# Performance work log

Hardware: AMD Instinct MI355X
Metric: run time of the kernel (lower is better)

## Reference

```python
import jax, jax.numpy as jnp
import numpy as np
from jax import tree_util as jtu

B, N, DIM = 2, 2048, 512
HEADS, DH = 4, 128
CHUNK = 64
NC = N // CHUNK
DHID = 4 * DH  # expansion_factor 4
MAX_LR = 1.0   # default_step_transform_max_lr


def rms_norm(x, g, eps=1e-6):
    var = jnp.mean(jnp.square(x), axis=-1, keepdims=True)
    return x * jax.lax.rsqrt(var + eps) * g


def mem_model(params, x):
    # ResidualNorm(MemoryMLP depth=2): out = mlp(rmsnorm(x)) + x
    g, w1, w2 = params
    h = rms_norm(x, g)
    h = jax.nn.gelu(jnp.dot(h, w1), approximate=False)
    h = jnp.dot(h, w2)
    return h + x


def _expand(a, leaf):
    # broadcast a per-(b*h) scalar gate over a weight leaf
    return a.reshape(a.shape + (1,) * (leaf.ndim - 1))


def neural_memory(seq, g_store, g_retrieve, Wq, Wk, Wv, Wa, ba, Wm, Wd, bd, Wg, Wc, mem_g, w1, w2):
    xs = rms_norm(seq, g_store)      # store_norm
    xr = rms_norm(seq, g_retrieve)   # retrieve_norm

    def split_heads(t):
        return t.reshape(B, N, HEADS, DH).transpose(0, 2, 1, 3)  # b h n d

    k = split_heads(xs @ Wk)
    v = split_heads(xs @ Wv)
    q = split_heads(xr @ Wq)

    # adaptive per-token lr (sigmoid * max_lr)
    lr = (jax.nn.sigmoid(xs @ Wa + ba) * MAX_LR).transpose(0, 2, 1)  # [B,H,N]
    # per-chunk pooled stats drive momentum + decay gates (AveragePool)
    pooled = xs.reshape(B, NC, CHUNK, DIM).mean(axis=2)              # [B,NC,DIM]
    beta = jax.nn.sigmoid(pooled @ Wm)                               # momentum factor [B,NC,H]
    alpha = 1.0 - jax.nn.sigmoid(pooled @ Wd + bd)                   # weight-retain (1-decay)

    BH = B * HEADS
    k_c = k.reshape(BH, NC, CHUNK, DH)
    v_c = v.reshape(BH, NC, CHUNK, DH)
    q_c = q.reshape(BH, NC, CHUNK, DH)
    lr_c = lr.reshape(BH, NC, CHUNK)
    beta_t = beta.transpose(0, 2, 1).reshape(BH, NC).T   # [NC,BH]
    alpha_t = alpha.transpose(0, 2, 1).reshape(BH, NC).T

    # per-head memory params repeated over batch*heads (per_head_learned_parameters)
    init_params = (
        jnp.broadcast_to(mem_g, (B, HEADS, DH)).reshape(BH, DH),
        jnp.broadcast_to(w1, (B, HEADS, DH, DHID)).reshape(BH, DH, DHID),
        jnp.broadcast_to(w2, (B, HEADS, DHID, DH)).reshape(BH, DHID, DH),
    )

    def chunk_loss(params, kc, vc, lrc):
        pred = mem_model(params, kc)                              # [CHUNK,DH]
        return jnp.sum(jnp.mean(jnp.square(pred - vc), axis=-1) * lrc)

    # per-chunk 'surprise' gradients: vmap over (b*h) and chunks, grads wrt init weights
    grad_fn = jax.grad(chunk_loss)
    grads = jax.vmap(jax.vmap(grad_fn, in_axes=(None, 0, 0, 0)), in_axes=(0, 0, 0, 0))(
        init_params, k_c, v_c, lr_c)
    sur_t = jtu.tree_map(lambda g: jnp.moveaxis(-g, 1, 0), grads)  # [NC,BH,...]

    # momentum recurrence: m_t = beta_t * m_{t-1} + surprise_t
    def mom_step(m, inp):
        b, s = inp
        m = jtu.tree_map(lambda mm, ss: _expand(b, mm) * mm + ss, m, s)
        return m, m
    m0 = jtu.tree_map(lambda t: jnp.zeros_like(t[0]), sur_t)
    _, upd_t = jax.lax.scan(mom_step, m0, (beta_t, sur_t))

    # weight recurrence with decay: w_t = (1-decay_t) * w_{t-1} + m_t
    def w_step(w, inp):
        a, u = inp
        w = jtu.tree_map(lambda ww, uu: _expand(a, ww) * ww + uu, w, u)
        return w, w
    _, w_t = jax.lax.scan(w_step, init_params, (alpha_t, upd_t))

    # causal retrieval: chunk i reads weights updated through chunk i-1
    w_prev = jtu.tree_map(
        lambda wt, w0: jnp.moveaxis(jnp.concatenate([w0[None], wt[:-1]], axis=0), 0, 1),
        w_t, init_params)                                          # [BH,NC,...]

    retrieved = jax.vmap(jax.vmap(mem_model))(w_prev, q_c)         # [BH,NC,CHUNK,DH]
    retrieved = retrieved.reshape(B, HEADS, N, DH)
    gate = jax.nn.sigmoid(xr @ Wg).transpose(0, 2, 1)[..., None]   # retrieve_gate [B,H,N,1]
    retrieved = retrieved * gate
    out = retrieved.transpose(0, 2, 1, 3).reshape(B, N, HEADS * DH) @ Wc  # combine_heads
    return out


def setup_inputs():
    key = jax.random.key(0)
    ks = jax.random.split(key, 12)
    s = 0.02
    f = jnp.float32
    return {
        "seq": jax.random.normal(ks[0], (B, N, DIM), f),
        "g_store": jnp.ones((DIM,), f),
        "g_retrieve": jnp.ones((DIM,), f),
        "Wq": jax.random.normal(ks[1], (DIM, HEADS * DH), f) * s,
        "Wk": jax.random.normal(ks[2], (DIM, HEADS * DH), f) * s,
        "Wv": jax.random.normal(ks[3], (DIM, HEADS * DH), f) * s,
        "Wa": jax.random.normal(ks[4], (DIM, HEADS), f) * s,
        "ba": jnp.zeros((HEADS,), f),
        "Wm": jax.random.normal(ks[5], (DIM, HEADS), f) * s,
        "Wd": jax.random.normal(ks[6], (DIM, HEADS), f) * s,
        "bd": jnp.zeros((HEADS,), f),
        "Wg": jax.random.normal(ks[7], (DIM, HEADS), f) * s,
        "Wc": jax.random.normal(ks[8], (HEADS * DH, DIM), f) * s,
        "mem_g": jnp.ones((DH,), f),
        "w1": jax.random.normal(ks[9], (DH, DHID), f) * (1.0 / np.sqrt(DH)),
        "w2": jax.random.normal(ks[10], (DHID, DH), f) * (1.0 / np.sqrt(DHID)),
    }


def reference(seq, g_store, g_retrieve, Wq, Wk, Wv, Wa, ba, Wm, Wd, bd, Wg, Wc, mem_g, w1, w2):
    return neural_memory(seq, g_store, g_retrieve, Wq, Wk, Wv, Wa, ba, Wm, Wd, bd, Wg, Wc, mem_g, w1, w2)
```

## Files before the change

### kernel.cpp

```cpp
#include <hip/hip_runtime.h>
#include <hip/hip_bf16.h>

#define B_ 2
#define N_ 2048
#define DIM_ 512
#define H_ 4
#define DH_ 128
#define DHID_ 512
#define CH_ 64
#define NC_ 32
#define BH_ 8

typedef __bf16 bf16x8 __attribute__((ext_vector_type(8)));
typedef float f32x4 __attribute__((ext_vector_type(4)));

__device__ __forceinline__ f32x4 MFMA(bf16x8 a, bf16x8 b, f32x4 c) {
    return __builtin_amdgcn_mfma_f32_16x16x32_bf16(a, b, c, 0, 0, 0);
}
__device__ __forceinline__ bf16x8 ld8(const __bf16* p) { return *(const bf16x8*)p; }

__device__ __forceinline__ float sigmoidf_(float x) { return 1.0f / (1.0f + expf(-x)); }
__device__ __forceinline__ float gelu_f(float x) {
    return x * 0.5f * (1.0f + erff(x * 0.7071067811865476f));
}
__device__ __forceinline__ float gelu_g(float x) {
    float cdf = 0.5f * (1.0f + erff(x * 0.7071067811865476f));
    float pdf = 0.3989422804014327f * expf(-0.5f * x * x);
    return cdf + x * pdf;
}

__global__ __launch_bounds__(256) void rms_kernel(
    const float* __restrict__ seq, const float* __restrict__ gs,
    const float* __restrict__ gr, float* __restrict__ xs, float* __restrict__ xr,
    __bf16* __restrict__ xsb, __bf16* __restrict__ xrb)
{
    const int row = blockIdx.x;
    const int t = threadIdx.x;
    const float* x = seq + (size_t)row * DIM_;
    float v0 = x[t], v1 = x[t + 256];
    float ss = v0 * v0 + v1 * v1;
#pragma unroll
    for (int off = 32; off; off >>= 1) ss += __shfl_xor(ss, off);
    __shared__ float red[4];
    if ((t & 63) == 0) red[t >> 6] = ss;
    __syncthreads();
    float tot = red[0] + red[1] + red[2] + red[3];
    float r = rsqrtf(tot * (1.0f / DIM_) + 1e-6f);
    size_t o = (size_t)row * DIM_;
    float a0 = v0 * r * gs[t], a1 = v1 * r * gs[t + 256];
    float b0 = v0 * r * gr[t], b1 = v1 * r * gr[t + 256];
    xs[o + t] = a0; xs[o + t + 256] = a1;
    xr[o + t] = b0; xr[o + t + 256] = b1;
    xsb[o + t] = (__bf16)a0; xsb[o + t + 256] = (__bf16)a1;
    xrb[o + t] = (__bf16)b0; xrb[o + t + 256] = (__bf16)b1;
}

__global__ __launch_bounds__(256) void pooled_kernel(
    const float* __restrict__ xs, float* __restrict__ pooled)
{
    int idx = blockIdx.x * 256 + threadIdx.x;
    int d = idx & 511;
    int ci = (idx >> 9) & 31;
    int b = idx >> 14;
    const float* base = xs + ((size_t)b * N_ + ci * CH_) * DIM_ + d;
    float s = 0.f;
#pragma unroll 8
    for (int c = 0; c < CH_; ++c) s += base[(size_t)c * DIM_];
    pooled[idx] = s * (1.0f / CH_);
}

__global__ __launch_bounds__(256) void gates_kernel(
    const float* __restrict__ xs, const float* __restrict__ xr,
    const float* __restrict__ Wa, const float* __restrict__ ba,
    const float* __restrict__ Wg, float* __restrict__ lrb, float* __restrict__ gateb)
{
    const int t = threadIdx.x;
    const int wave = t >> 6, lane = t & 63;
    const int row = blockIdx.x * 4 + wave;
    const int b = row >> 11, n = row & 2047;
    const float* xsr = xs + (size_t)row * DIM_;
    const float* xrr = xr + (size_t)row * DIM_;
#pragma unroll
    for (int h = 0; h < H_; ++h) {
        float aA = 0.f, aG = 0.f;
        for (int d = lane; d < DIM_; d += 64) {
            aA += xsr[d] * Wa[d * H_ + h];
            aG += xrr[d] * Wg[d * H_ + h];
        }
#pragma unroll
        for (int off = 32; off; off >>= 1) {
            aA += __shfl_xor(aA, off);
            aG += __shfl_xor(aG, off);
        }
        if (lane == 0) {
            int bh = b * H_ + h;
            lrb[(size_t)bh * N_ + n] = sigmoidf_(aA + ba[h]);
            gateb[(size_t)bh * N_ + n] = sigmoidf_(aG);
        }
    }
}

__global__ __launch_bounds__(256) void ba_kernel(
    const float* __restrict__ pooled, const float* __restrict__ Wm,
    const float* __restrict__ Wd, const float* __restrict__ bd,
    float* __restrict__ beta, float* __restrict__ alpha)
{
    const int t = threadIdx.x;
    const int b = t >> 7, rem = t & 127, ci = rem >> 2, h = rem & 3;
    const float* p = pooled + ((size_t)b * NC_ + ci) * DIM_;
    float am = 0.f, ad = 0.f;
    for (int d = 0; d < DIM_; ++d) {
        float pv = p[d];
        am += pv * Wm[d * H_ + h];
        ad += pv * Wd[d * H_ + h];
    }
    int bh = b * H_ + h;
    beta[bh * NC_ + ci] = sigmoidf_(am);
    alpha[bh * NC_ + ci] = 1.0f - sigmoidf_(ad + bd[h]);
}

__global__ __launch_bounds__(256) void prep_kernel(
    const float* __restrict__ w1, const float* __restrict__ w2,
    const float* __restrict__ Wq, const float* __restrict__ Wk,
    const float* __restrict__ Wv, const float* __restrict__ Wc,
    __bf16* __restrict__ w1b, __bf16* __restrict__ w1Tb,
    __bf16* __restrict__ w2b, __bf16* __restrict__ w2Tb,
    __bf16* __restrict__ WqT, __bf16* __restrict__ WkT,
    __bf16* __restrict__ WvT, __bf16* __restrict__ WcT)
{
    int idx = blockIdx.x * 256 + threadIdx.x;
    if (idx < 65536) {
        w1b[idx] = (__bf16)w1[idx];
        int j = idx >> 7, d = idx & 127;
        w1Tb[idx] = (__bf16)w1[(size_t)d * DHID_ + j];
        w2b[idx] = (__bf16)w2[idx];
        int d2 = idx >> 9, j2 = idx & 511;
        w2Tb[idx] = (__bf16)w2[(size_t)j2 * DH_ + d2];
    }
    int n = idx >> 9, k = idx & 511;
    WqT[idx] = (__bf16)Wq[(size_t)k * 512 + n];
    WkT[idx] = (__bf16)Wk[(size_t)k * 512 + n];
    WvT[idx] = (__bf16)Wv[(size_t)k * 512 + n];
    WcT[idx] = (__bf16)Wc[(size_t)k * 512 + n];
}

template <int SPLIT>
__global__ __launch_bounds__(256, 4) void gemm_bf(
    const __bf16* __restrict__ A, const __bf16* __restrict__ WT, float* __restrict__ out)
{
    const int t = threadIdx.x;
    const int wave = t >> 6, lane = t & 63;
    const int lrow = lane & 15, lgrp = lane >> 4;
    const int c0 = blockIdx.x * 64 + wave * 16;
    const int col0 = blockIdx.y * 64;
    f32x4 acc[4];
#pragma unroll
    for (int i = 0; i < 4; ++i) acc[i] = (f32x4)0.f;
    const __bf16* ar = A + (size_t)(c0 + lrow) * 512;
#pragma unroll 4
    for (int k0 = 0; k0 < 512; k0 += 32) {
        bf16x8 av = ld8(ar + k0 + lgrp * 8);
#pragma unroll
        for (int ct = 0; ct < 4; ++ct) {
            bf16x8 bv = ld8(WT + (size_t)(col0 + ct * 16 + lrow) * 512 + k0 + lgrp * 8);
            acc[ct] = MFMA(av, bv, acc[ct]);
        }
    }
#pragma unroll
    for (int ct = 0; ct < 4; ++ct)
#pragma unroll
        for (int r = 0; r < 4; ++r) {
            int row = c0 + lgrp * 4 + r, col = col0 + ct * 16 + lrow;
            if (SPLIT) {
                int b = row >> 11, n = row & 2047, h = col >> 7, d = col & 127;
                out[((((size_t)(b * H_ + h) * NC_ + (n >> 6)) * CH_) + (n & 63)) * DH_ + d] = acc[ct][r];
            } else {
                out[(size_t)row * 512 + col] = acc[ct][r];
            }
        }
}

__global__ __launch_bounds__(512, 2) void grad_kernel(
    const float* __restrict__ kbuf, const float* __restrict__ vbuf,
    const float* __restrict__ lrbuf, const float* __restrict__ memg,
    const __bf16* __restrict__ w1b, const __bf16* __restrict__ w1Tb,
    const __bf16* __restrict__ w2b, const __bf16* __restrict__ w2Tb,
    float* __restrict__ sg, __bf16* __restrict__ sw1, __bf16* __restrict__ sw2)
{
    const int blk = blockIdx.x;
    const int t = threadIdx.x;
    const int w = t >> 6, lane = t & 63;
    const int lrow = lane & 15, lgrp = lane >> 4;
    const int bh = blk >> 5, nc = blk & 31;
    const float* kc = kbuf + (size_t)blk * (CH_ * DH_);
    const float* vc = vbuf + (size_t)blk * (CH_ * DH_);
    const float* lrp = lrbuf + (size_t)bh * N_ + nc * CH_;
    __bf16* sw1_blk = sw1 + (size_t)blk * (DHID_ * DH_);
    __bf16* sw2_blk = sw2 + (size_t)blk * (DHID_ * DH_);

    __shared__ __bf16 h_s[64][136];
    __shared__ __bf16 e_s[64][136];
    __shared__ __bf16 a_s[64][136];
    __shared__ __bf16 dz_s[64][136];
    __shared__ __bf16 hT_s[128][72];
    __shared__ __bf16 eT_s[128][72];
    __shared__ __bf16 aT_s[128][72];
    __shared__ __bf16 dzT_s[128][72];
    __shared__ float r_s[64];
    __shared__ float lr_s[64];
    __shared__ float g_s[128];

    if (t < 128) g_s[t] = memg[t];
    if (t < 64) lr_s[t] = lrp[t];
    {
        const int c = t >> 3, dblk = t & 7, d0 = dblk * 16;
        float xv[16];
        float ss = 0.f;
#pragma unroll
        for (int i = 0; i < 4; ++i) {
            float4 f = *(const float4*)(kc + (size_t)c * DH_ + d0 + i * 4);
            xv[i * 4 + 0] = f.x; xv[i * 4 + 1] = f.y; xv[i * 4 + 2] = f.z; xv[i * 4 + 3] = f.w;
            ss += f.x * f.x + f.y * f.y + f.z * f.z + f.w * f.w;
        }
        ss += __shfl_xor(ss, 1); ss += __shfl_xor(ss, 2); ss += __shfl_xor(ss, 4);
        float r = rsqrtf(ss * (1.0f / DH_) + 1e-6f);
        if (dblk == 0) r_s[c] = r;
        __syncthreads();
#pragma unroll
        for (int i = 0; i < 16; ++i)
            h_s[c][d0 + i] = (__bf16)(xv[i] * r * g_s[d0 + i]);
    }
    __syncthreads();
    {
        const int d = t >> 2, c0 = (t & 3) * 16;
#pragma unroll
        for (int i = 0; i < 16; ++i) hT_s[d][c0 + i] = h_s[c0 + i][d];
    }
    __syncthreads();

    const int cs = w & 3, half = w >> 2;
    const int c0w = cs * 16, off64 = half * 64;
    f32x4 yacc[4];
#pragma unroll
    for (int i = 0; i < 4; ++i) yacc[i] = (f32x4)0.f;

    for (int jt = 0; jt < 4; ++jt) {
        f32x4 zacc[4];
#pragma unroll
        for (int i = 0; i < 4; ++i) zacc[i] = (f32x4)0.f;
#pragma unroll
        for (int kt = 0; kt < 4; ++kt) {
            bf16x8 av = ld8(&h_s[c0w + lrow][kt * 32 + lgrp * 8]);
#pragma unroll
            for (int ct = 0; ct < 4; ++ct) {
                int j = jt * 128 + off64 + ct * 16 + lrow;
                bf16x8 bv = ld8(w1Tb + (size_t)j * 128 + kt * 32 + lgrp * 8);
                zacc[ct] = MFMA(av, bv, zacc[ct]);
            }
        }
#pragma unroll
        for (int ct = 0; ct < 4; ++ct)
#pragma unroll
            for (int r = 0; r < 4; ++r)
                a_s[c0w + lgrp * 4 + r][off64 + ct * 16 + lrow] = (__bf16)gelu_f(zacc[ct][r]);
        __syncthreads();
#pragma unroll
        for (int kt = 0; kt < 4; ++kt) {
            bf16x8 av = ld8(&a_s[c0w + lrow][kt * 32 + lgrp * 8]);
#pragma unroll
            for (int ct = 0; ct < 4; ++ct) {
                int d = off64 + ct * 16 + lrow;
                bf16x8 bv = ld8(w2Tb + (size_t)d * 512 + jt * 128 + kt * 32 + lgrp * 8);
                yacc[ct] = MFMA(av, bv, yacc[ct]);
            }
        }
        __syncthreads();
    }
#pragma unroll
    for (int ct = 0; ct < 4; ++ct)
#pragma unroll
        for (int r = 0; r < 4; ++r) {
            int c = c0w + lgrp * 4 + r, d = off64 + ct * 16 + lrow;
            float xvv = kc[(size_t)c * DH_ + d];
            float vvv = vc[(size_t)c * DH_ + d];
            float e = lr_s[c] * (2.0f / DH_) * (yacc[ct][r] + xvv - vvv);
            e_s[c][d] = (__bf16)e;
            eT_s[d][c] = (__bf16)e;
        }
    __syncthreads();

    const int jl0 = w * 16;
    f32x4 dhacc[4];
#pragma unroll
    for (int i = 0; i < 4; ++i) dhacc[i] = (f32x4)0.f;

    for (int jt = 0; jt < 4; ++jt) {
        f32x4 ztacc[4], dtacc[4];
#pragma unroll
        for (int i = 0; i < 4; ++i) { ztacc[i] = (f32x4)0.f; dtacc[i] = (f32x4)0.f; }
#pragma unroll
        for (int kt = 0; kt < 4; ++kt) {
            bf16x8 avz = ld8(w1Tb + (size_t)(jt * 128 + jl0 + lrow) * 128 + kt * 32 + lgrp * 8);
            bf16x8 avd = ld8(w2b  + (size_t)(jt * 128 + jl0 + lrow) * 128 + kt * 32 + lgrp * 8);
#pragma unroll
            for (int ct = 0; ct < 4; ++ct) {
                bf16x8 bvh = ld8(&h_s[ct * 16 + lrow][kt * 32 + lgrp * 8]);
                bf16x8 bve = ld8(&e_s[ct * 16 + lrow][kt * 32 + lgrp * 8]);
                ztacc[ct] = MFMA(avz, bvh, ztacc[ct]);
                dtacc[ct] = MFMA(avd, bve, dtacc[ct]);
            }
        }
#pragma unroll
        for (int ct = 0; ct < 4; ++ct)
#pragma unroll
            for (int r = 0; r < 4; ++r) {
                int j = jl0 + lgrp * 4 + r, c = ct * 16 + lrow;
                float zt = ztacc[ct][r];
                aT_s[j][c] = (__bf16)gelu_f(zt);
                float dzt = dtacc[ct][r] * gelu_g(zt);
                dzT_s[j][c] = (__bf16)dzt;
                dz_s[c][j] = (__bf16)dzt;
            }
        __syncthreads();
        {
            f32x4 wacc[8];
#pragma unroll
            for (int i = 0; i < 8; ++i) wacc[i] = (f32x4)0.f;
#pragma unroll
            for (int kt = 0; kt < 2; ++kt) {
                bf16x8 av = ld8(&dzT_s[jl0 + lrow][kt * 32 + lgrp * 8]);
#pragma unroll
                for (int ct = 0; ct < 8; ++ct) {
                    bf16x8 bv = ld8(&hT_s[ct * 16 + lrow][kt * 32 + lgrp * 8]);
                    wacc[ct] = MFMA(av, bv, wacc[ct]);
                }
            }
#pragma unroll
            for (int ct = 0; ct < 8; ++ct)
#pragma unroll
                for (int r = 0; r < 4; ++r) {
                    int jg = jt * 128 + jl0 + lgrp * 4 + r, d = ct * 16 + lrow;
                    sw1_blk[(size_t)jg * 128 + d] = (__bf16)(-wacc[ct][r]);
                }
        }
        {
            f32x4 wacc[8];
#pragma unroll
            for (int i = 0; i < 8; ++i) wacc[i] = (f32x4)0.f;
#pragma unroll
            for (int kt = 0; kt < 2; ++kt) {
                bf16x8 av = ld8(&eT_s[jl0 + lrow][kt * 32 + lgrp * 8]);
#pragma unroll
                for (int ct = 0; ct < 8; ++ct) {
                    bf16x8 bv = ld8(&aT_s[ct * 16 + lrow][kt * 32 + lgrp * 8]);
                    wacc[ct] = MFMA(av, bv, wacc[ct]);
                }
            }
#pragma unroll
            for (int ct = 0; ct < 8; ++ct)
#pragma unroll
                for (int r = 0; r < 4; ++r) {
                    int d = jl0 + lgrp * 4 + r, jg = jt * 128 + ct * 16 + lrow;
                    sw2_blk[(size_t)d * 512 + jg] = (__bf16)(-wacc[ct][r]);
                }
        }
#pragma unroll
        for (int kt = 0; kt < 4; ++kt) {
            bf16x8 av = ld8(w1b + (size_t)(jl0 + lrow) * 512 + jt * 128 + kt * 32 + lgrp * 8);
#pragma unroll
            for (int ct = 0; ct < 4; ++ct) {
                bf16x8 bv = ld8(&dz_s[ct * 16 + lrow][kt * 32 + lgrp * 8]);
                dhacc[ct] = MFMA(av, bv, dhacc[ct]);
            }
        }
        __syncthreads();
    }
    {
        float s[4] = {0.f, 0.f, 0.f, 0.f};
#pragma unroll
        for (int ct = 0; ct < 4; ++ct)
#pragma unroll
            for (int r = 0; r < 4; ++r) {
                int d = jl0 + lgrp * 4 + r, c = ct * 16 + lrow;
                s[r] += dhacc[ct][r] * (float)hT_s[d][c];
            }
#pragma unroll
        for (int r = 0; r < 4; ++r) {
            s[r] += __shfl_xor(s[r], 1); s[r] += __shfl_xor(s[r], 2);
            s[r] += __shfl_xor(s[r], 4); s[r] += __shfl_xor(s[r], 8);
        }
        if (lrow == 0) {
#pragma unroll
            for (int r = 0; r < 4; ++r) {
                int d = jl0 + lgrp * 4 + r;
                sg[(size_t)blk * DH_ + d] = -s[r] / g_s[d];
            }
        }
    }
}

__global__ __launch_bounds__(256) void scan_bf(
    __bf16* __restrict__ buf, const __bf16* __restrict__ init,
    const float* __restrict__ beta, const float* __restrict__ alpha)
{
    int idx = blockIdx.x * 256 + threadIdx.x;
    int bh = idx >> 16, el = idx & 65535;
    float wv = (float)init[el], m = 0.f;
    const float* bp = beta + bh * NC_;
    const float* ap = alpha + bh * NC_;
    __bf16* base = buf + ((size_t)bh * NC_) * 65536 + el;
    for (int ci = 0; ci < NC_; ++ci) {
        float s = (float)base[(size_t)ci * 65536];
        base[(size_t)ci * 65536] = (__bf16)wv;
        m = fmaf(bp[ci], m, s);
        wv = fmaf(ap[ci], wv, m);
    }
}

__global__ __launch_bounds__(256) void scan_g(
    float* __restrict__ buf, const float* __restrict__ init,
    const float* __restrict__ beta, const float* __restrict__ alpha)
{
    int idx = blockIdx.x * 256 + threadIdx.x;
    int bh = idx >> 7, el = idx & 127;
    float wv = init[el], m = 0.f;
    const float* bp = beta + bh * NC_;
    const float* ap = alpha + bh * NC_;
    float* base = buf + ((size_t)bh * NC_) * 128 + el;
    for (int ci = 0; ci < NC_; ++ci) {
        float s = base[(size_t)ci * 128];
        base[(size_t)ci * 128] = wv;
        m = fmaf(bp[ci], m, s);
        wv = fmaf(ap[ci], wv, m);
    }
}

__global__ __launch_bounds__(256, 2) void retrieve_kernel(
    const float* __restrict__ qbuf, const float* __restrict__ gatebuf,
    const float* __restrict__ sg, const __bf16* __restrict__ sw1,
    const __bf16* __restrict__ sw2, __bf16* __restrict__ retgb)
{
    const int blk = blockIdx.x;
    const int t = threadIdx.x;
    const int w = t >> 6, lane = t & 63;
    const int lrow = lane & 15, lgrp = lane >> 4;
    const int bh = blk >> 5, nc = blk & 31;
    const float* qc = qbuf + (size_t)blk * (CH_ * DH_);
    const __bf16* w1p = sw1 + (size_t)blk * (DHID_ * DH_);
    const __bf16* w2p = sw2 + (size_t)blk * (DHID_ * DH_);
    const float* gp = sg + (size_t)blk * DH_;

    __shared__ __bf16 h_s[64][136];
    __shared__ __bf16 a_s[64][136];
    __shared__ float g_s[128];

    if (t < 128) g_s[t] = gp[t];
    {
        const int c = t >> 2, dblk = t & 3, d0 = dblk * 32;
        float xv[32];
        float ss = 0.f;
#pragma unroll
        for (int i = 0; i < 8; ++i) {
            float4 f = *(const float4*)(qc + (size_t)c * DH_ + d0 + i * 4);
            xv[i * 4 + 0] = f.x; xv[i * 4 + 1] = f.y; xv[i * 4 + 2] = f.z; xv[i * 4 + 3] = f.w;
            ss += f.x * f.x + f.y * f.y + f.z * f.z + f.w * f.w;
        }
        ss += __shfl_xor(ss, 1); ss += __shfl_xor(ss, 2);
        float r = rsqrtf(ss * (1.0f / DH_) + 1e-6f);
        __syncthreads();
#pragma unroll
        for (int i = 0; i < 32; ++i)
            h_s[c][d0 + i] = (__bf16)(xv[i] * r * g_s[d0 + i]);
    }
    __syncthreads();

    const int c0w = w * 16;
    f32x4 yacc[8];
#pragma unroll
    for (int i = 0; i < 8; ++i) yacc[i] = (f32x4)0.f;

    for (int jt = 0; jt < 4; ++jt) {
        f32x4 zacc[8];
#pragma unroll
        for (int i = 0; i < 8; ++i) zacc[i] = (f32x4)0.f;
#pragma unroll
        for (int kt = 0; kt < 4; ++kt) {
            bf16x8 av = ld8(&h_s[c0w + lrow][kt * 32 + lgrp * 8]);
#pragma unroll
            for (int ct = 0; ct < 8; ++ct) {
                int j = jt * 128 + ct * 16 + lrow;
                bf16x8 bv = ld8(w1p + (size_t)j * 128 + kt * 32 + lgrp * 8);
                zacc[ct] = MFMA(av, bv, zacc[ct]);
            }
        }
#pragma unroll
        for (int ct = 0; ct < 8; ++ct)
#pragma unroll
            for (int r = 0; r < 4; ++r)
                a_s[c0w + lgrp * 4 + r][ct * 16 + lrow] = (__bf16)gelu_f(zacc[ct][r]);
        __syncthreads();
#pragma unroll
        for (int kt = 0; kt < 4; ++kt) {
            bf16x8 av = ld8(&a_s[c0w + lrow][kt * 32 + lgrp * 8]);
#pragma unroll
            for (int ct = 0; ct < 8; ++ct) {
                int d = ct * 16 + lrow;
                bf16x8 bv = ld8(w2p + (size_t)d * 512 + jt * 128 + kt * 32 + lgrp * 8);
                yacc[ct] = MFMA(av, bv, yacc[ct]);
            }
        }
        __syncthreads();
    }
    const int b = bh >> 2, hh = bh & 3;
#pragma unroll
    for (int ct = 0; ct < 8; ++ct)
#pragma unroll
        for (int r = 0; r < 4; ++r) {
            int c = c0w + lgrp * 4 + r, d = ct * 16 + lrow;
            int n = nc * CH_ + c;
            float q = qc[(size_t)c * DH_ + d];
            float gv = gatebuf[(size_t)bh * N_ + n];
            retgb[((size_t)(b * N_ + n)) * 512 + hh * 128 + d] = (__bf16)((yacc[ct][r] + q) * gv);
        }
}

extern "C" void kernel_launch(void* const* d_in, const int* in_sizes, int n_in,
                              void* d_out, int out_size, void* d_ws, size_t ws_size,
                              hipStream_t stream) {
    const float* seq     = (const float*)d_in[0];
    const float* g_store = (const float*)d_in[1];
    const float* g_retr  = (const float*)d_in[2];
    const float* Wq = (const float*)d_in[3];
    const float* Wk = (const float*)d_in[4];
    const float* Wv = (const float*)d_in[5];
    const float* Wa = (const float*)d_in[6];
    const float* ba = (const float*)d_in[7];
    const float* Wm = (const float*)d_in[8];
    const float* Wd = (const float*)d_in[9];
    const float* bd = (const float*)d_in[10];
    const float* Wg = (const float*)d_in[11];
    const float* Wc = (const float*)d_in[12];
    const float* memg = (const float*)d_in[13];
    const float* w1 = (const float*)d_in[14];
    const float* w2 = (const float*)d_in[15];
    float* out = (float*)d_out;

    float* p = (float*)d_ws;
    float* xs = p;     p += (size_t)B_ * N_ * DIM_;
    float* xr = p;     p += (size_t)B_ * N_ * DIM_;
    float* kb = p;     p += (size_t)B_ * N_ * DIM_;
    float* vb = p;     p += (size_t)B_ * N_ * DIM_;
    float* qb = p;     p += (size_t)B_ * N_ * DIM_;
    float* lrb = p;    p += (size_t)BH_ * N_;
    float* gateb = p;  p += (size_t)BH_ * N_;
    float* pooled = p; p += (size_t)B_ * NC_ * DIM_;
    float* beta = p;   p += BH_ * NC_;
    float* alpha = p;  p += BH_ * NC_;
    float* sgb = p;    p += (size_t)BH_ * NC_ * DH_;

    __bf16* bp_ = (__bf16*)p;
    __bf16* xsb = bp_;  bp_ += (size_t)B_ * N_ * DIM_;
    __bf16* xrb = bp_;  bp_ += (size_t)B_ * N_ * DIM_;
    __bf16* retgb = bp_; bp_ += (size_t)B_ * N_ * DIM_;
    __bf16* w1b = bp_;  bp_ += DH_ * DHID_;
    __bf16* w1Tb = bp_; bp_ += DH_ * DHID_;
    __bf16* w2b = bp_;  bp_ += DH_ * DHID_;
    __bf16* w2Tb = bp_; bp_ += DH_ * DHID_;
    __bf16* WqT = bp_;  bp_ += DIM_ * DIM_;
    __bf16* WkT = bp_;  bp_ += DIM_ * DIM_;
    __bf16* WvT = bp_;  bp_ += DIM_ * DIM_;
    __bf16* WcT = bp_;  bp_ += DIM_ * DIM_;
    __bf16* sw1b = bp_; bp_ += (size_t)BH_ * NC_ * DH_ * DHID_;
    __bf16* sw2b = bp_; bp_ += (size_t)BH_ * NC_ * DH_ * DHID_;

    rms_kernel<<<B_ * N_, 256, 0, stream>>>(seq, g_store, g_retr, xs, xr, xsb, xrb);
    pooled_kernel<<<(B_ * NC_ * DIM_) / 256, 256, 0, stream>>>(xs, pooled);
    gates_kernel<<<(B_ * N_) / 4, 256, 0, stream>>>(xs, xr, Wa, ba, Wg, lrb, gateb);
    ba_kernel<<<1, 256, 0, stream>>>(pooled, Wm, Wd, bd, beta, alpha);
    prep_kernel<<<1024, 256, 0, stream>>>(w1, w2, Wq, Wk, Wv, Wc,
                                          w1b, w1Tb, w2b, w2Tb, WqT, WkT, WvT, WcT);
    gemm_bf<1><<<dim3(64, 8), 256, 0, stream>>>(xrb, WqT, qb);
    gemm_bf<1><<<dim3(64, 8), 256, 0, stream>>>(xsb, WkT, kb);
    gemm_bf<1><<<dim3(64, 8), 256, 0, stream>>>(xsb, WvT, vb);
    grad_kernel<<<BH_ * NC_, 512, 0, stream>>>(kb, vb, lrb, memg, w1b, w1Tb, w2b, w2Tb,
                                               sgb, sw1b, sw2b);
    scan_bf<<<(BH_ * 65536) / 256, 256, 0, stream>>>(sw1b, w1Tb, beta, alpha);
    scan_bf<<<(BH_ * 65536) / 256, 256, 0, stream>>>(sw2b, w2Tb, beta, alpha);
    scan_g<<<(BH_ * DH_) / 256, 256, 0, stream>>>(sgb, memg, beta, alpha);
    retrieve_kernel<<<BH_ * NC_, 256, 0, stream>>>(qb, gateb, sgb, sw1b, sw2b, retgb);
    gemm_bf<0><<<dim3(64, 8), 256, 0, stream>>>(retgb, WcT, out);
}
```

Before: 387.2 us.

## Fuse small kernels and double threads per block in grad and retrieve

Folds the lr/gate projections into the RMS-norm kernel, and merges the pooling with the beta/alpha gates into one kernel that runs on 64 blocks instead of one. The three QKV GEMMs become one launch over a z grid dimension, and the three scan launches become one. grad_kernel moves from 512 to 1024 threads and retrieve_kernel from 256 to 512, with each wave taking a smaller tile so only 256 blocks spread more work across waves. This cuts launch count and raises per-block parallelism, at the cost of more per-thread register pressure limits and extra synchronisation.

```diff
diff --git a/kernel.cpp b/kernel.cpp
--- a/kernel.cpp
+++ b/kernel.cpp
@@ -31,18 +31,23 @@
 
 __global__ __launch_bounds__(256) void rms_kernel(
     const float* __restrict__ seq, const float* __restrict__ gs,
-    const float* __restrict__ gr, float* __restrict__ xs, float* __restrict__ xr,
-    __bf16* __restrict__ xsb, __bf16* __restrict__ xrb)
+    const float* __restrict__ gr, const float* __restrict__ Wa,
+    const float* __restrict__ ba, const float* __restrict__ Wg,
+    float* __restrict__ xs, float* __restrict__ xr,
+    __bf16* __restrict__ xsb, __bf16* __restrict__ xrb,
+    float* __restrict__ lrb, float* __restrict__ gateb)
 {
     const int row = blockIdx.x;
     const int t = threadIdx.x;
+    const int wave = t >> 6, lane = t & 63;
     const float* x = seq + (size_t)row * DIM_;
     float v0 = x[t], v1 = x[t + 256];
     float ss = v0 * v0 + v1 * v1;
 #pragma unroll
     for (int off = 32; off; off >>= 1) ss += __shfl_xor(ss, off);
     __shared__ float red[4];
-    if ((t & 63) == 0) red[t >> 6] = ss;
+    __shared__ float red2[4][8];
+    if (lane == 0) red[wave] = ss;
     __syncthreads();
     float tot = red[0] + red[1] + red[2] + red[3];
     float r = rsqrtf(tot * (1.0f / DIM_) + 1e-6f);
@@ -53,70 +58,81 @@
     xr[o + t] = b0; xr[o + t + 256] = b1;
     xsb[o + t] = (__bf16)a0; xsb[o + t + 256] = (__bf16)a1;
     xrb[o + t] = (__bf16)b0; xrb[o + t + 256] = (__bf16)b1;
-}
-
-__global__ __launch_bounds__(256) void pooled_kernel(
-    const float* __restrict__ xs, float* __restrict__ pooled)
-{
-    int idx = blockIdx.x * 256 + threadIdx.x;
-    int d = idx & 511;
-    int ci = (idx >> 9) & 31;
-    int b = idx >> 14;
-    const float* base = xs + ((size_t)b * N_ + ci * CH_) * DIM_ + d;
-    float s = 0.f;
-#pragma unroll 8
-    for (int c = 0; c < CH_; ++c) s += base[(size_t)c * DIM_];
-    pooled[idx] = s * (1.0f / CH_);
-}
-
-__global__ __launch_bounds__(256) void gates_kernel(
-    const float* __restrict__ xs, const float* __restrict__ xr,
-    const float* __restrict__ Wa, const float* __restrict__ ba,
-    const float* __restrict__ Wg, float* __restrict__ lrb, float* __restrict__ gateb)
-{
+    float pa[4], pg[4];
+#pragma unroll
+    for (int h = 0; h < 4; ++h) {
+        pa[h] = a0 * Wa[t * 4 + h] + a1 * Wa[(t + 256) * 4 + h];
+        pg[h] = b0 * Wg[t * 4 + h] + b1 * Wg[(t + 256) * 4 + h];
+    }
+#pragma unroll
+    for (int h = 0; h < 4; ++h)
+#pragma unroll
+        for (int off = 32; off; off >>= 1) {
+            pa[h] += __shfl_xor(pa[h], off);
+            pg[h] += __shfl_xor(pg[h], off);
+        }
+    if (lane == 0) {
+#pragma unroll
+        for (int h = 0; h < 4; ++h) {
+            red2[wave][h] = pa[h];
+            red2[wave][4 + h] = pg[h];
+        }
+    }
+    __syncthreads();
+    if (t < 8) {
+        float s = red2[0][t] + red2[1][t] + red2[2][t] + red2[3][t];
+        int b = row >> 11, n = row & 2047;
+        if (t < 4) lrb[(size_t)(b * 4 + t) * N_ + n] = sigmoidf_(s + ba[t]);
+        else gateb[(size_t)(b * 4 + (t - 4)) * N_ + n] = sigmoidf_(s);
+    }
+}
+
+__global__ __launch_bounds__(256) void ba_kernel(
+    const float* __restrict__ xs, const float* __restrict__ Wm,
+    const float* __restrict__ Wd, const float* __restrict__ bd,
+    float* __restrict__ beta, float* __restrict__ alpha)
+{
+    const int b = blockIdx.x >> 5, ci = blockIdx.x & 31;
     const int t = threadIdx.x;
     const int wave = t >> 6, lane = t & 63;
-    const int row = blockIdx.x * 4 + wave;
-    const int b = row >> 11, n = row & 2047;
-    const float* xsr = xs + (size_t)row * DIM_;
-    const float* xrr = xr + (size_t)row * DIM_;
-#pragma unroll
-    for (int h = 0; h < H_; ++h) {
-        float aA = 0.f, aG = 0.f;
-        for (int d = lane; d < DIM_; d += 64) {
-            aA += xsr[d] * Wa[d * H_ + h];
-            aG += xrr[d] * Wg[d * H_ + h];
-        }
+    const float* base = xs + ((size_t)b * N_ + ci * CH_) * DIM_;
+    const int d0 = t * 2;
+    float s0 = 0.f, s1 = 0.f;
+#pragma unroll 8
+    for (int r = 0; r < CH_; ++r) {
+        s0 += base[(size_t)r * DIM_ + d0];
+        s1 += base[(size_t)r * DIM_ + d0 + 1];
+    }
+    s0 *= (1.0f / CH_); s1 *= (1.0f / CH_);
+    float pm[4], pd[4];
+#pragma unroll
+    for (int h = 0; h < 4; ++h) {
+        pm[h] = s0 * Wm[d0 * 4 + h] + s1 * Wm[(d0 + 1) * 4 + h];
+        pd[h] = s0 * Wd[d0 * 4 + h] + s1 * Wd[(d0 + 1) * 4 + h];
+    }
+#pragma unroll
+    for (int h = 0; h < 4; ++h)
 #pragma unroll
         for (int off = 32; off; off >>= 1) {
-            aA += __shfl_xor(aA, off);
-            aG += __shfl_xor(aG, off);
-        }
-        if (lane == 0) {
-            int bh = b * H_ + h;
-            lrb[(size_t)bh * N_ + n] = sigmoidf_(aA + ba[h]);
-            gateb[(size_t)bh * N_ + n] = sigmoidf_(aG);
-        }
-    }
-}
-
-__global__ __launch_bounds__(256) void ba_kernel(
-    const float* __restrict__ pooled, const float* __restrict__ Wm,
-    const float* __restrict__ Wd, const float* __restrict__ bd,
-    float* __restrict__ beta, float* __restrict__ alpha)
-{
-    const int t = threadIdx.x;
-    const int b = t >> 7, rem = t & 127, ci = rem >> 2, h = rem & 3;
-    const float* p = pooled + ((size_t)b * NC_ + ci) * DIM_;
-    float am = 0.f, ad = 0.f;
-    for (int d = 0; d < DIM_; ++d) {
-        float pv = p[d];
-        am += pv * Wm[d * H_ + h];
-        ad += pv * Wd[d * H_ + h];
-    }
-    int bh = b * H_ + h;
-    beta[bh * NC_ + ci] = sigmoidf_(am);
-    alpha[bh * NC_ + ci] = 1.0f - sigmoidf_(ad + bd[h]);
+            pm[h] += __shfl_xor(pm[h], off);
+            pd[h] += __shfl_xor(pd[h], off);
+        }
+    __shared__ float red2[4][8];
+    if (lane == 0) {
+#pragma unroll
+        for (int h = 0; h < 4; ++h) {
+            red2[wave][h] = pm[h];
+            red2[wave][4 + h] = pd[h];
+        }
+    }
+    __syncthreads();
+    if (t < 4) {
+        float sm = red2[0][t] + red2[1][t] + red2[2][t] + red2[3][t];
+        float sd = red2[0][4 + t] + red2[1][4 + t] + red2[2][4 + t] + red2[3][4 + t];
+        int bh = b * 4 + t;
+        beta[bh * NC_ + ci] = sigmoidf_(sm);
+        alpha[bh * NC_ + ci] = 1.0f - sigmoidf_(sd + bd[t]);
+    }
 }
 
 __global__ __launch_bounds__(256) void prep_kernel(
@@ -144,10 +160,16 @@
     WcT[idx] = (__bf16)Wc[(size_t)k * 512 + n];
 }
 
-template <int SPLIT>
-__global__ __launch_bounds__(256, 4) void gemm_bf(
-    const __bf16* __restrict__ A, const __bf16* __restrict__ WT, float* __restrict__ out)
-{
+__global__ __launch_bounds__(256, 4) void proj_kernel(
+    const __bf16* __restrict__ xsb, const __bf16* __restrict__ xrb,
+    const __bf16* __restrict__ WqT, const __bf16* __restrict__ WkT,
+    const __bf16* __restrict__ WvT,
+    float* __restrict__ qb, float* __restrict__ kb, float* __restrict__ vb)
+{
+    const int z = blockIdx.z;
+    const __bf16* A = (z == 0) ? xrb : xsb;
+    const __bf16* WT = (z == 0) ? WqT : (z == 1 ? WkT : WvT);
+    float* out = (z == 0) ? qb : (z == 1 ? kb : vb);
     const int t = threadIdx.x;
     const int wave = t >> 6, lane = t & 63;
     const int lrow = lane & 15, lgrp = lane >> 4;
@@ -171,16 +193,42 @@
 #pragma unroll
         for (int r = 0; r < 4; ++r) {
             int row = c0 + lgrp * 4 + r, col = col0 + ct * 16 + lrow;
-            if (SPLIT) {
-                int b = row >> 11, n = row & 2047, h = col >> 7, d = col & 127;
-                out[((((size_t)(b * H_ + h) * NC_ + (n >> 6)) * CH_) + (n & 63)) * DH_ + d] = acc[ct][r];
-            } else {
-                out[(size_t)row * 512 + col] = acc[ct][r];
-            }
-        }
-}
-
-__global__ __launch_bounds__(512, 2) void grad_kernel(
+            int b = row >> 11, n = row & 2047, h = col >> 7, d = col & 127;
+            out[((((size_t)(b * H_ + h) * NC_ + (n >> 6)) * CH_) + (n & 63)) * DH_ + d] = acc[ct][r];
+        }
+}
+
+__global__ __launch_bounds__(256, 4) void gemm_out(
+    const __bf16* __restrict__ A, const __bf16* __restrict__ WT, float* __restrict__ out)
+{
+    const int t = threadIdx.x;
+    const int wave = t >> 6, lane = t & 63;
+    const int lrow = lane & 15, lgrp = lane >> 4;
+    const int c0 = blockIdx.x * 64 + wave * 16;
+    const int col0 = blockIdx.y * 64;
+    f32x4 acc[4];
+#pragma unroll
+    for (int i = 0; i < 4; ++i) acc[i] = (f32x4)0.f;
+    const __bf16* ar = A + (size_t)(c0 + lrow) * 512;
+#pragma unroll 4
+    for (int k0 = 0; k0 < 512; k0 += 32) {
+        bf16x8 av = ld8(ar + k0 + lgrp * 8);
+#pragma unroll
+        for (int ct = 0; ct < 4; ++ct) {
+            bf16x8 bv = ld8(WT + (size_t)(col0 + ct * 16 + lrow) * 512 + k0 + lgrp * 8);
+            acc[ct] = MFMA(av, bv, acc[ct]);
+        }
+    }
+#pragma unroll
+    for (int ct = 0; ct < 4; ++ct)
+#pragma unroll
+        for (int r = 0; r < 4; ++r) {
+            int row = c0 + lgrp * 4 + r, col = col0 + ct * 16 + lrow;
+            out[(size_t)row * 512 + col] = acc[ct][r];
+        }
+}
+
+__global__ __launch_bounds__(1024) void grad_kernel(
     const float* __restrict__ kbuf, const float* __restrict__ vbuf,
     const float* __restrict__ lrbuf, const float* __restrict__ memg,
     const __bf16* __restrict__ w1b, const __bf16* __restrict__ w1Tb,
@@ -209,67 +257,67 @@
     __shared__ float r_s[64];
     __shared__ float lr_s[64];
     __shared__ float g_s[128];
+    __shared__ float part_s[2][128];
 
     if (t < 128) g_s[t] = memg[t];
     if (t < 64) lr_s[t] = lrp[t];
     {
-        const int c = t >> 3, dblk = t & 7, d0 = dblk * 16;
-        float xv[16];
+        const int c = t >> 4, i8 = t & 15, d0 = i8 * 8;
+        float xv[8];
         float ss = 0.f;
 #pragma unroll
-        for (int i = 0; i < 4; ++i) {
+        for (int i = 0; i < 2; ++i) {
             float4 f = *(const float4*)(kc + (size_t)c * DH_ + d0 + i * 4);
             xv[i * 4 + 0] = f.x; xv[i * 4 + 1] = f.y; xv[i * 4 + 2] = f.z; xv[i * 4 + 3] = f.w;
             ss += f.x * f.x + f.y * f.y + f.z * f.z + f.w * f.w;
         }
-        ss += __shfl_xor(ss, 1); ss += __shfl_xor(ss, 2); ss += __shfl_xor(ss, 4);
+        ss += __shfl_xor(ss, 1); ss += __shfl_xor(ss, 2);
+        ss += __shfl_xor(ss, 4); ss += __shfl_xor(ss, 8);
         float r = rsqrtf(ss * (1.0f / DH_) + 1e-6f);
-        if (dblk == 0) r_s[c] = r;
-        __syncthreads();
-#pragma unroll
-        for (int i = 0; i < 16; ++i)
+        if (i8 == 0) r_s[c] = r;
+        __syncthreads();
+#pragma unroll
+        for (int i = 0; i < 8; ++i)
             h_s[c][d0 + i] = (__bf16)(xv[i] * r * g_s[d0 + i]);
     }
     __syncthreads();
     {
-        const int d = t >> 2, c0 = (t & 3) * 16;
-#pragma unroll
-        for (int i = 0; i < 16; ++i) hT_s[d][c0 + i] = h_s[c0 + i][d];
+        const int d = t >> 3, c0 = (t & 7) * 8;
+#pragma unroll
+        for (int i = 0; i < 8; ++i) hT_s[d][c0 + i] = h_s[c0 + i][d];
     }
     __syncthreads();
 
-    const int cs = w & 3, half = w >> 2;
-    const int c0w = cs * 16, off64 = half * 64;
-    f32x4 yacc[4];
-#pragma unroll
-    for (int i = 0; i < 4; ++i) yacc[i] = (f32x4)0.f;
+    const int cs = w & 3, dq = w >> 2;
+    const int c0w = cs * 16, q0 = dq * 32;
+    f32x4 yacc[2];
+    yacc[0] = (f32x4)0.f; yacc[1] = (f32x4)0.f;
 
     for (int jt = 0; jt < 4; ++jt) {
-        f32x4 zacc[4];
-#pragma unroll
-        for (int i = 0; i < 4; ++i) zacc[i] = (f32x4)0.f;
+        f32x4 zacc[2];
+        zacc[0] = (f32x4)0.f; zacc[1] = (f32x4)0.f;
 #pragma unroll
         for (int kt = 0; kt < 4; ++kt) {
             bf16x8 av = ld8(&h_s[c0w + lrow][kt * 32 + lgrp * 8]);
 #pragma unroll
-            for (int ct = 0; ct < 4; ++ct) {
-                int j = jt * 128 + off64 + ct * 16 + lrow;
+            for (int ct = 0; ct < 2; ++ct) {
+                int j = jt * 128 + q0 + ct * 16 + lrow;
                 bf16x8 bv = ld8(w1Tb + (size_t)j * 128 + kt * 32 + lgrp * 8);
                 zacc[ct] = MFMA(av, bv, zacc[ct]);
             }
         }
 #pragma unroll
-        for (int ct = 0; ct < 4; ++ct)
+        for (int ct = 0; ct < 2; ++ct)
 #pragma unroll
             for (int r = 0; r < 4; ++r)
-                a_s[c0w + lgrp * 4 + r][off64 + ct * 16 + lrow] = (__bf16)gelu_f(zacc[ct][r]);
+                a_s[c0w + lgrp * 4 + r][q0 + ct * 16 + lrow] = (__bf16)gelu_f(zacc[ct][r]);
         __syncthreads();
 #pragma unroll
         for (int kt = 0; kt < 4; ++kt) {
             bf16x8 av = ld8(&a_s[c0w + lrow][kt * 32 + lgrp * 8]);
 #pragma unroll
-            for (int ct = 0; ct < 4; ++ct) {
-                int d = off64 + ct * 16 + lrow;
+            for (int ct = 0; ct < 2; ++ct) {
+                int d = q0 + ct * 16 + lrow;
                 bf16x8 bv = ld8(w2Tb + (size_t)d * 512 + jt * 128 + kt * 32 + lgrp * 8);
                 yacc[ct] = MFMA(av, bv, yacc[ct]);
             }
@@ -277,10 +325,10 @@
         __syncthreads();
     }
 #pragma unroll
-    for (int ct = 0; ct < 4; ++ct)
+    for (int ct = 0; ct < 2; ++ct)
 #pragma unroll
         for (int r = 0; r < 4; ++r) {
-            int c = c0w + lgrp * 4 + r, d = off64 + ct * 16 + lrow;
+            int c = c0w + lgrp * 4 + r, d = q0 + ct * 16 + lrow;
             float xvv = kc[(size_t)c * DH_ + d];
             float vvv = vc[(size_t)c * DH_ + d];
             float e = lr_s[c] * (2.0f / DH_) * (yacc[ct][r] + xvv - vvv);
@@ -289,32 +337,31 @@
         }
     __syncthreads();
 
-    const int jl0 = w * 16;
-    f32x4 dhacc[4];
-#pragma unroll
-    for (int i = 0; i < 4; ++i) dhacc[i] = (f32x4)0.f;
+    const int js = w & 7, chh = w >> 3;
+    f32x4 dhacc[2];
+    dhacc[0] = (f32x4)0.f; dhacc[1] = (f32x4)0.f;
 
     for (int jt = 0; jt < 4; ++jt) {
-        f32x4 ztacc[4], dtacc[4];
-#pragma unroll
-        for (int i = 0; i < 4; ++i) { ztacc[i] = (f32x4)0.f; dtacc[i] = (f32x4)0.f; }
+        f32x4 ztacc[2], dtacc[2];
+        ztacc[0] = (f32x4)0.f; ztacc[1] = (f32x4)0.f;
+        dtacc[0] = (f32x4)0.f; dtacc[1] = (f32x4)0.f;
 #pragma unroll
         for (int kt = 0; kt < 4; ++kt) {
-            bf16x8 avz = ld8(w1Tb + (size_t)(jt * 128 + jl0 + lrow) * 128 + kt * 32 + lgrp * 8);
-            bf16x8 avd = ld8(w2b  + (size_t)(jt * 128 + jl0 + lrow) * 128 + kt * 32 + lgrp * 8);
-#pragma unroll
-            for (int ct = 0; ct < 4; ++ct) {
-                bf16x8 bvh = ld8(&h_s[ct * 16 + lrow][kt * 32 + lgrp * 8]);
-                bf16x8 bve = ld8(&e_s[ct * 16 + lrow][kt * 32 + lgrp * 8]);
+            bf16x8 avz = ld8(w1Tb + (size_t)(jt * 128 + js * 16 + lrow) * 128 + kt * 32 + lgrp * 8);
+            bf16x8 avd = ld8(w2b  + (size_t)(jt * 128 + js * 16 + lrow) * 128 + kt * 32 + lgrp * 8);
+#pragma unroll
+            for (int ct = 0; ct < 2; ++ct) {
+                bf16x8 bvh = ld8(&h_s[chh * 32 + ct * 16 + lrow][kt * 32 + lgrp * 8]);
+                bf16x8 bve = ld8(&e_s[chh * 32 + ct * 16 + lrow][kt * 32 + lgrp * 8]);
                 ztacc[ct] = MFMA(avz, bvh, ztacc[ct]);
                 dtacc[ct] = MFMA(avd, bve, dtacc[ct]);
             }
         }
 #pragma unroll
-        for (int ct = 0; ct < 4; ++ct)
+        for (int ct = 0; ct < 2; ++ct)
 #pragma unroll
             for (int r = 0; r < 4; ++r) {
-                int j = jl0 + lgrp * 4 + r, c = ct * 16 + lrow;
+                int j = js * 16 + lgrp * 4 + r, c = chh * 32 + ct * 16 + lrow;
                 float zt = ztacc[ct][r];
                 aT_s[j][c] = (__bf16)gelu_f(zt);
                 float dzt = dtacc[ct][r] * gelu_g(zt);
@@ -323,53 +370,53 @@
             }
         __syncthreads();
         {
-            f32x4 wacc[8];
-#pragma unroll
-            for (int i = 0; i < 8; ++i) wacc[i] = (f32x4)0.f;
+            f32x4 wacc[4];
+#pragma unroll
+            for (int i = 0; i < 4; ++i) wacc[i] = (f32x4)0.f;
 #pragma unroll
             for (int kt = 0; kt < 2; ++kt) {
-                bf16x8 av = ld8(&dzT_s[jl0 + lrow][kt * 32 + lgrp * 8]);
-#pragma unroll
-                for (int ct = 0; ct < 8; ++ct) {
-                    bf16x8 bv = ld8(&hT_s[ct * 16 + lrow][kt * 32 + lgrp * 8]);
+                bf16x8 av = ld8(&dzT_s[js * 16 + lrow][kt * 32 + lgrp * 8]);
+#pragma unroll
+                for (int ct = 0; ct < 4; ++ct) {
+                    bf16x8 bv = ld8(&hT_s[chh * 64 + ct * 16 + lrow][kt * 32 + lgrp * 8]);
                     wacc[ct] = MFMA(av, bv, wacc[ct]);
                 }
             }
 #pragma unroll
-            for (int ct = 0; ct < 8; ++ct)
+            for (int ct = 0; ct < 4; ++ct)
 #pragma unroll
                 for (int r = 0; r < 4; ++r) {
-                    int jg = jt * 128 + jl0 + lgrp * 4 + r, d = ct * 16 + lrow;
+                    int jg = jt * 128 + js * 16 + lgrp * 4 + r, d = chh * 64 + ct * 16 + lrow;
                     sw1_blk[(size_t)jg * 128 + d] = (__bf16)(-wacc[ct][r]);
                 }
         }
         {
-            f32x4 wacc[8];
-#pragma unroll
-            for (int i = 0; i < 8; ++i) wacc[i] = (f32x4)0.f;
+            f32x4 wacc[4];
+#pragma unroll
+            for (int i = 0; i < 4; ++i) wacc[i] = (f32x4)0.f;
 #pragma unroll
             for (int kt = 0; kt < 2; ++kt) {
-                bf16x8 av = ld8(&eT_s[jl0 + lrow][kt * 32 + lgrp * 8]);
-#pragma unroll
-                for (int ct = 0; ct < 8; ++ct) {
-                    bf16x8 bv = ld8(&aT_s[ct * 16 + lrow][kt * 32 + lgrp * 8]);
+                bf16x8 av = ld8(&eT_s[js * 16 + lrow][kt * 32 + lgrp * 8]);
+#pragma unroll
+                for (int ct = 0; ct < 4; ++ct) {
+                    bf16x8 bv = ld8(&aT_s[chh * 64 + ct * 16 + lrow][kt * 32 + lgrp * 8]);
                     wacc[ct] = MFMA(av, bv, wacc[ct]);
                 }
             }
 #pragma unroll
-            for (int ct = 0; ct < 8; ++ct)
+            for (int ct = 0; ct < 4; ++ct)
 #pragma unroll
                 for (int r = 0; r < 4; ++r) {
-                    int d = jl0 + lgrp * 4 + r, jg = jt * 128 + ct * 16 + lrow;
+                    int d = js * 16 + lgrp * 4 + r, jg = jt * 128 + chh * 64 + ct * 16 + lrow;
                     sw2_blk[(size_t)d * 512 + jg] = (__bf16)(-wacc[ct][r]);
                 }
         }
 #pragma unroll
         for (int kt = 0; kt < 4; ++kt) {
-            bf16x8 av = ld8(w1b + (size_t)(jl0 + lrow) * 512 + jt * 128 + kt * 32 + lgrp * 8);
-#pragma unroll
-            for (int ct = 0; ct < 4; ++ct) {
-                bf16x8 bv = ld8(&dz_s[ct * 16 + lrow][kt * 32 + lgrp * 8]);
+            bf16x8 av = ld8(w1b + (size_t)(js * 16 + lrow) * 512 + jt * 128 + kt * 32 + lgrp * 8);
+#pragma unroll
+            for (int ct = 0; ct < 2; ++ct) {
+                bf16x8 bv = ld8(&dz_s[chh * 32 + ct * 16 + lrow][kt * 32 + lgrp * 8]);
                 dhacc[ct] = MFMA(av, bv, dhacc[ct]);
             }
         }
@@ -378,10 +425,10 @@
     {
         float s[4] = {0.f, 0.f, 0.f, 0.f};
 #pragma unroll
-        for (int ct = 0; ct < 4; ++ct)
+        for (int ct = 0; ct < 2; ++ct)
 #pragma unroll
             for (int r = 0; r < 4; ++r) {
-                int d = jl0 + lgrp * 4 + r, c = ct * 16 + lrow;
+                int d = js * 16 + lgrp * 4 + r, c = chh * 32 + ct * 16 + lrow;
                 s[r] += dhacc[ct][r] * (float)hT_s[d][c];
             }
 #pragma unroll
@@ -391,51 +438,52 @@
         }
         if (lrow == 0) {
 #pragma unroll
-            for (int r = 0; r < 4; ++r) {
-                int d = jl0 + lgrp * 4 + r;
-                sg[(size_t)blk * DH_ + d] = -s[r] / g_s[d];
-            }
-        }
-    }
-}
-
-__global__ __launch_bounds__(256) void scan_bf(
-    __bf16* __restrict__ buf, const __bf16* __restrict__ init,
+            for (int r = 0; r < 4; ++r) part_s[chh][js * 16 + lgrp * 4 + r] = s[r];
+        }
+        __syncthreads();
+        if (t < 128) sg[(size_t)blk * DH_ + t] = -(part_s[0][t] + part_s[1][t]) / g_s[t];
+    }
+}
+
+__global__ __launch_bounds__(256) void scan_all(
+    __bf16* __restrict__ sw1, const __bf16* __restrict__ w1T,
+    __bf16* __restrict__ sw2, const __bf16* __restrict__ w2T,
+    float* __restrict__ sgb, const float* __restrict__ memg,
     const float* __restrict__ beta, const float* __restrict__ alpha)
 {
-    int idx = blockIdx.x * 256 + threadIdx.x;
-    int bh = idx >> 16, el = idx & 65535;
-    float wv = (float)init[el], m = 0.f;
-    const float* bp = beta + bh * NC_;
-    const float* ap = alpha + bh * NC_;
-    __bf16* base = buf + ((size_t)bh * NC_) * 65536 + el;
-    for (int ci = 0; ci < NC_; ++ci) {
-        float s = (float)base[(size_t)ci * 65536];
-        base[(size_t)ci * 65536] = (__bf16)wv;
-        m = fmaf(bp[ci], m, s);
-        wv = fmaf(ap[ci], wv, m);
-    }
-}
-
-__global__ __launch_bounds__(256) void scan_g(
-    float* __restrict__ buf, const float* __restrict__ init,
-    const float* __restrict__ beta, const float* __restrict__ alpha)
-{
-    int idx = blockIdx.x * 256 + threadIdx.x;
-    int bh = idx >> 7, el = idx & 127;
-    float wv = init[el], m = 0.f;
-    const float* bp = beta + bh * NC_;
-    const float* ap = alpha + bh * NC_;
-    float* base = buf + ((size_t)bh * NC_) * 128 + el;
-    for (int ci = 0; ci < NC_; ++ci) {
-        float s = base[(size_t)ci * 128];
-        base[(size_t)ci * 128] = wv;
-        m = fmaf(bp[ci], m, s);
-        wv = fmaf(ap[ci], wv, m);
-    }
-}
-
-__global__ __launch_bounds__(256, 2) void retrieve_kernel(
+    const int bi = blockIdx.x, t = threadIdx.x;
+    if (bi < 4096) {
+        __bf16* buf = (bi < 2048) ? sw1 : sw2;
+        const __bf16* init = (bi < 2048) ? w1T : w2T;
+        int idx = (bi & 2047) * 256 + t;
+        int bh = idx >> 16, el = idx & 65535;
+        float wv = (float)init[el], m = 0.f;
+        const float* bp = beta + bh * NC_;
+        const float* ap = alpha + bh * NC_;
+        __bf16* base = buf + ((size_t)bh * NC_) * 65536 + el;
+        for (int ci = 0; ci < NC_; ++ci) {
+            float s = (float)base[(size_t)ci * 65536];
+            base[(size_t)ci * 65536] = (__bf16)wv;
+            m = fmaf(bp[ci], m, s);
+            wv = fmaf(ap[ci], wv, m);
+        }
+    } else {
+        int idx = (bi - 4096) * 256 + t;
+        int bh = idx >> 7, el = idx & 127;
+        float wv = memg[el], m = 0.f;
+        const float* bp = beta + bh * NC_;
+        const float* ap = alpha + bh * NC_;
+        float* base = sgb + ((size_t)bh * NC_) * 128 + el;
+        for (int ci = 0; ci < NC_; ++ci) {
+            float s = base[(size_t)ci * 128];
+            base[(size_t)ci * 128] = wv;
+            m = fmaf(bp[ci], m, s);
+            wv = fmaf(ap[ci], wv, m);
+        }
+    }
+}
+
+__global__ __launch_bounds__(512, 4) void retrieve_kernel(
     const float* __restrict__ qbuf, const float* __restrict__ gatebuf,
     const float* __restrict__ sg, const __bf16* __restrict__ sw1,
     const __bf16* __restrict__ sw2, __bf16* __restrict__ retgb)
@@ -456,55 +504,56 @@
 
     if (t < 128) g_s[t] = gp[t];
     {
-        const int c = t >> 2, dblk = t & 3, d0 = dblk * 32;
-        float xv[32];
+        const int c = t >> 3, dblk = t & 7, d0 = dblk * 16;
+        float xv[16];
         float ss = 0.f;
 #pragma unroll
-        for (int i = 0; i < 8; ++i) {
+        for (int i = 0; i < 4; ++i) {
             float4 f = *(const float4*)(qc + (size_t)c * DH_ + d0 + i * 4);
             xv[i * 4 + 0] = f.x; xv[i * 4 + 1] = f.y; xv[i * 4 + 2] = f.z; xv[i * 4 + 3] = f.w;
             ss += f.x * f.x + f.y * f.y + f.z * f.z + f.w * f.w;
         }
-        ss += __shfl_xor(ss, 1); ss += __shfl_xor(ss, 2);
+        ss += __shfl_xor(ss, 1); ss += __shfl_xor(ss, 2); ss += __shfl_xor(ss, 4);
         float r = rsqrtf(ss * (1.0f / DH_) + 1e-6f);
         __syncthreads();
 #pragma unroll
-        for (int i = 0; i < 32; ++i)
+        for (int i = 0; i < 16; ++i)
             h_s[c][d0 + i] = (__bf16)(xv[i] * r * g_s[d0 + i]);
     }
     __syncthreads();
 
-    const int c0w = w * 16;
-    f32x4 yacc[8];
-#pragma unroll
-    for (int i = 0; i < 8; ++i) yacc[i] = (f32x4)0.f;
+    const int cs = w & 3, dh2 = w >> 2;
+    const int c0w = cs * 16, d0w = dh2 * 64;
+    f32x4 yacc[4];
+#pragma unroll
+    for (int i = 0; i < 4; ++i) yacc[i] = (f32x4)0.f;
 
     for (int jt = 0; jt < 4; ++jt) {
-        f32x4 zacc[8];
-#pragma unroll
-        for (int i = 0; i < 8; ++i) zacc[i] = (f32x4)0.f;
+        f32x4 zacc[4];
+#pragma unroll
+        for (int i = 0; i < 4; ++i) zacc[i] = (f32x4)0.f;
 #pragma unroll
         for (int kt = 0; kt < 4; ++kt) {
             bf16x8 av = ld8(&h_s[c0w + lrow][kt * 32 + lgrp * 8]);
 #pragma unroll
-            for (int ct = 0; ct < 8; ++ct) {
-                int j = jt * 128 + ct * 16 + lrow;
+            for (int ct = 0; ct < 4; ++ct) {
+                int j = jt * 128 + d0w + ct * 16 + lrow;
                 bf16x8 bv = ld8(w1p + (size_t)j * 128 + kt * 32 + lgrp * 8);
                 zacc[ct] = MFMA(av, bv, zacc[ct]);
             }
         }
 #pragma unroll
-        for (int ct = 0; ct < 8; ++ct)
+        for (int ct = 0; ct < 4; ++ct)
 #pragma unroll
             for (int r = 0; r < 4; ++r)
-                a_s[c0w + lgrp * 4 + r][ct * 16 + lrow] = (__bf16)gelu_f(zacc[ct][r]);
+                a_s[c0w + lgrp * 4 + r][d0w + ct * 16 + lrow] = (__bf16)gelu_f(zacc[ct][r]);
         __syncthreads();
 #pragma unroll
         for (int kt = 0; kt < 4; ++kt) {
             bf16x8 av = ld8(&a_s[c0w + lrow][kt * 32 + lgrp * 8]);
 #pragma unroll
-            for (int ct = 0; ct < 8; ++ct) {
-                int d = ct * 16 + lrow;
+            for (int ct = 0; ct < 4; ++ct) {
+                int d = d0w + ct * 16 + lrow;
                 bf16x8 bv = ld8(w2p + (size_t)d * 512 + jt * 128 + kt * 32 + lgrp * 8);
                 yacc[ct] = MFMA(av, bv, yacc[ct]);
             }
@@ -513,10 +562,10 @@
     }
     const int b = bh >> 2, hh = bh & 3;
 #pragma unroll
-    for (int ct = 0; ct < 8; ++ct)
+    for (int ct = 0; ct < 4; ++ct)
 #pragma unroll
         for (int r = 0; r < 4; ++r) {
-            int c = c0w + lgrp * 4 + r, d = ct * 16 + lrow;
+            int c = c0w + lgrp * 4 + r, d = d0w + ct * 16 + lrow;
             int n = nc * CH_ + c;
             float q = qc[(size_t)c * DH_ + d];
             float gv = gatebuf[(size_t)bh * N_ + n];
@@ -553,7 +602,6 @@
     float* qb = p;     p += (size_t)B_ * N_ * DIM_;
     float* lrb = p;    p += (size_t)BH_ * N_;
     float* gateb = p;  p += (size_t)BH_ * N_;
-    float* pooled = p; p += (size_t)B_ * NC_ * DIM_;
     float* beta = p;   p += BH_ * NC_;
     float* alpha = p;  p += BH_ * NC_;
     float* sgb = p;    p += (size_t)BH_ * NC_ * DH_;
@@ -573,20 +621,15 @@
     __bf16* sw1b = bp_; bp_ += (size_t)BH_ * NC_ * DH_ * DHID_;
     __bf16* sw2b = bp_; bp_ += (size_t)BH_ * NC_ * DH_ * DHID_;
 
-    rms_kernel<<<B_ * N_, 256, 0, stream>>>(seq, g_store, g_retr, xs, xr, xsb, xrb);
-    pooled_kernel<<<(B_ * NC_ * DIM_) / 256, 256, 0, stream>>>(xs, pooled);
-    gates_kernel<<<(B_ * N_) / 4, 256, 0, stream>>>(xs, xr, Wa, ba, Wg, lrb, gateb);
-    ba_kernel<<<1, 256, 0, stream>>>(pooled, Wm, Wd, bd, beta, alpha);
+    rms_kernel<<<B_ * N_, 256, 0, stream>>>(seq, g_store, g_retr, Wa, ba, Wg,
+                                            xs, xr, xsb, xrb, lrb, gateb);
+    ba_kernel<<<B_ * NC_, 256, 0, stream>>>(xs, Wm, Wd, bd, beta, alpha);
     prep_kernel<<<1024, 256, 0, stream>>>(w1, w2, Wq, Wk, Wv, Wc,
                                           w1b, w1Tb, w2b, w2Tb, WqT, WkT, WvT, WcT);
-    gemm_bf<1><<<dim3(64, 8), 256, 0, stream>>>(xrb, WqT, qb);
-    gemm_bf<1><<<dim3(64, 8), 256, 0, stream>>>(xsb, WkT, kb);
-    gemm_bf<1><<<dim3(64, 8), 256, 0, stream>>>(xsb, WvT, vb);
-    grad_kernel<<<BH_ * NC_, 512, 0, stream>>>(kb, vb, lrb, memg, w1b, w1Tb, w2b, w2Tb,
-                                               sgb, sw1b, sw2b);
-    scan_bf<<<(BH_ * 65536) / 256, 256, 0, stream>>>(sw1b, w1Tb, beta, alpha);
-    scan_bf<<<(BH_ * 65536) / 256, 256, 0, stream>>>(sw2b, w2Tb, beta, alpha);
-    scan_g<<<(BH_ * DH_) / 256, 256, 0, stream>>>(sgb, memg, beta, alpha);
-    retrieve_kernel<<<BH_ * NC_, 256, 0, stream>>>(qb, gateb, sgb, sw1b, sw2b, retgb);
-    gemm_bf<0><<<dim3(64, 8), 256, 0, stream>>>(retgb, WcT, out);
-}
+    proj_kernel<<<dim3(64, 8, 3), 256, 0, stream>>>(xsb, xrb, WqT, WkT, WvT, qb, kb, vb);
+    grad_kernel<<<BH_ * NC_, 1024, 0, stream>>>(kb, vb, lrb, memg, w1b, w1Tb, w2b, w2Tb,
+                                                sgb, sw1b, sw2b);
+    scan_all<<<4100, 256, 0, stream>>>(sw1b, w1Tb, sw2b, w2Tb, sgb, memg, beta, alpha);
+    retrieve_kernel<<<BH_ * NC_, 512, 0, stream>>>(qb, gateb, sgb, sw1b, sw2b, retgb);
+    gemm_out<<<dim3(64, 8), 256, 0, stream>>>(retgb, WcT, out);
+}
```

Measured after the change: 336.0 us. -13.2%, faster.
